# Optimization experiments

Hardware: AMD Instinct MI355X
Metric: run time of the kernel (lower is better)

## Reference

```python
import jax, jax.numpy as jnp
import numpy as np

N, LQ, C = 8, 5440, 256
NH, NL, NP = 8, 4, 4
D_FFN = 1024
SHAPES = np.array([[64, 64], [32, 32], [16, 16], [8, 8]], dtype=np.int32)  # (H, W) per level
assert SHAPES.prod(1).sum() == LQ


def setup_inputs() -> dict:
    key = jax.random.key(0)
    ks = jax.random.split(key, 12)
    s = 0.02
    level_start = np.concatenate([[0], np.cumsum(SHAPES.prod(1))[:-1]]).astype(np.int32)
    return {
        "src": jax.random.normal(ks[0], (N, LQ, C), jnp.float32),
        "pos": jax.random.normal(ks[1], (N, LQ, C), jnp.float32),
        "reference_points": jax.random.uniform(ks[2], (N, LQ, NL, 2), jnp.float32),
        "w_off": jax.random.normal(ks[3], (C, NH * NL * NP * 2), jnp.float32) * s,
        "b_off": jax.random.uniform(ks[4], (NH * NL * NP * 2,), jnp.float32, -0.5, 0.5),
        "w_attn": jax.random.normal(ks[5], (C, NH * NL * NP), jnp.float32) * s,
        "b_attn": jnp.zeros((NH * NL * NP,), jnp.float32),
        "w_val": jax.random.normal(ks[6], (C, C), jnp.float32) * s,
        "b_val": jnp.zeros((C,), jnp.float32),
        "w_out": jax.random.normal(ks[7], (C, C), jnp.float32) * s,
        "b_out": jnp.zeros((C,), jnp.float32),
        "g1": jnp.ones((C,), jnp.float32),
        "be1": jnp.zeros((C,), jnp.float32),
        "w_ff1": jax.random.normal(ks[8], (C, D_FFN), jnp.float32) * s,
        "b_ff1": jnp.zeros((D_FFN,), jnp.float32),
        "w_ff2": jax.random.normal(ks[9], (D_FFN, C), jnp.float32) * s,
        "b_ff2": jnp.zeros((C,), jnp.float32),
        "g2": jnp.ones((C,), jnp.float32),
        "be2": jnp.zeros((C,), jnp.float32),
        "padding_mask": jnp.zeros((N, LQ), bool),
        "spatial_shapes": jnp.asarray(SHAPES),
        "level_start_index": jnp.asarray(level_start),
    }


def _layer_norm(x, g, b, eps=1e-5):
    m = x.mean(-1, keepdims=True)
    v = ((x - m) ** 2).mean(-1, keepdims=True)
    return (x - m) / jnp.sqrt(v + eps) * g + b


def _bilinear(v, gx, gy, Hl, Wl):
    # v: [B, Hl*Wl, D]; gx, gy: [B, Q] normalized grid coords in [-1, 1].
    # Matches F.grid_sample(mode='bilinear', padding_mode='zeros', align_corners=False).
    x = (gx + 1.0) * (Wl * 0.5) - 0.5
    y = (gy + 1.0) * (Hl * 0.5) - 0.5
    x0f, y0f = jnp.floor(x), jnp.floor(y)
    wx, wy = x - x0f, y - y0f
    x0, y0 = x0f.astype(jnp.int32), y0f.astype(jnp.int32)

    def corner(xi, yi, w):
        valid = (xi >= 0) & (xi < Wl) & (yi >= 0) & (yi < Hl)
        idx = jnp.clip(yi, 0, Hl - 1) * Wl + jnp.clip(xi, 0, Wl - 1)
        g = jnp.take_along_axis(v, idx[..., None], axis=1)  # [B, Q, D]
        return g * (w * valid)[..., None]

    return (corner(x0, y0, (1 - wx) * (1 - wy))
            + corner(x0 + 1, y0, wx * (1 - wy))
            + corner(x0, y0 + 1, (1 - wx) * wy)
            + corner(x0 + 1, y0 + 1, wx * wy))


def _forward(src, pos, reference_points, w_off, b_off, w_attn, b_attn, w_val, b_val,
             w_out, b_out, g1, be1, w_ff1, b_ff1, w_ff2, b_ff2, g2, be2, padding_mask):
    D = C // NH
    query = src + pos  # with_pos_embed
    # --- MSDeformAttn ---
    value = src @ w_val + b_val
    value = jnp.where(padding_mask[..., None], 0.0, value).reshape(N, LQ, NH, D)
    off = (query @ w_off + b_off).reshape(N, LQ, NH, NL, NP, 2)
    aw = jax.nn.softmax((query @ w_attn + b_attn).reshape(N, LQ, NH, NL * NP), axis=-1)
    aw = aw.reshape(N, LQ, NH, NL, NP)
    wh = jnp.asarray(SHAPES[:, ::-1].copy(), jnp.float32)  # (W, H) per level
    loc = reference_points[:, :, None, :, None, :] + off / wh[None, None, None, :, None, :]
    out = jnp.zeros((N, LQ, NH, D), src.dtype)
    start = 0
    for l in range(NL):
        Hl, Wl = int(SHAPES[l, 0]), int(SHAPES[l, 1])
        # [N, HW_l, NH, D] -> [N*NH, HW_l, D]
        v = value[:, start:start + Hl * Wl].transpose(0, 2, 1, 3).reshape(N * NH, Hl * Wl, D)
        g = (2.0 * loc[:, :, :, l] - 1.0).transpose(0, 2, 1, 3, 4).reshape(N * NH, LQ * NP, 2)
        samp = _bilinear(v, g[..., 0], g[..., 1], Hl, Wl).reshape(N, NH, LQ, NP, D)
        out = out + jnp.einsum('nhqpd,nqhp->nqhd', samp, aw[:, :, :, l])
        start += Hl * Wl
    src2 = out.reshape(N, LQ, C) @ w_out + b_out
    # --- residual + norm + FFN (dropout = identity in eval) ---
    x = _layer_norm(src + src2, g1, be1)
    h = jax.nn.relu(x @ w_ff1 + b_ff1)
    x = _layer_norm(x + h @ w_ff2 + b_ff2, g2, be2)
    return x


def reference(src, pos, reference_points, w_off, b_off, w_attn, b_attn, w_val, b_val,
              w_out, b_out, g1, be1, w_ff1, b_ff1, w_ff2, b_ff2, g2, be2,
              padding_mask, spatial_shapes, level_start_index):
    return _forward(src, pos, reference_points, w_off, b_off, w_attn, b_attn, w_val, b_val,
                    w_out, b_out, g1, be1, w_ff1, b_ff1, w_ff2, b_ff2, g2, be2, padding_mask)
```

## Files before the change

### kernel.cpp

```cpp
#include <hip/hip_runtime.h>
#include <hip/hip_bf16.h>

typedef __hip_bfloat16 bf16;
typedef __attribute__((ext_vector_type(8))) short short8;
typedef __attribute__((ext_vector_type(4))) float f32x4;

#define NB    8
#define LQ    5440
#define CCH   256
#define NHD   8
#define DFF   1024
#define TT    (NB * LQ)

__device__ __forceinline__ float b2f(bf16 x) { return __bfloat162float(x); }
__device__ __forceinline__ bf16  f2b(float x) { return __float2bfloat16(x); }

__device__ __forceinline__ void gl_lds16(const bf16* g, bf16* l) {
    __builtin_amdgcn_global_load_lds(
        (const __attribute__((address_space(1))) unsigned int*)g,
        (__attribute__((address_space(3))) unsigned int*)l,
        16, 0, 0);
}

template <bool RELU, bool OUT_BF16>
__global__ __launch_bounds__(256) void mfma_gemm(
    const bf16* __restrict__ A, const bf16* __restrict__ BT,
    const float* __restrict__ bias, void* __restrict__ Cout,
    int M, int N, int K)
{
    __shared__ bf16 Abuf[128 * 32];
    __shared__ bf16 Bbuf[128 * 32];

    const int tid = threadIdx.x;
    const int wv = tid >> 6;
    const int ln = tid & 63;
    const int lane15 = ln & 15;
    const int quad = ln >> 4;
    const int m0 = blockIdx.y * 128;
    const int n0 = blockIdx.x * 128;
    const int wm = (wv >> 1) * 64;
    const int wn = (wv & 1) * 64;

    const int ar = tid >> 2;
    const int ac = (tid & 3) * 8;

    const bf16* gA = A  + (size_t)(m0 + ar) * K + ac;
    const bf16* gB = BT + (size_t)(n0 + ar) * K + ac;

    f32x4 acc[4][4];
#pragma unroll
    for (int i = 0; i < 4; i++)
#pragma unroll
        for (int j = 0; j < 4; j++) acc[i][j] = (f32x4){0.f, 0.f, 0.f, 0.f};

    const int KT = K >> 5;
    for (int kt = 0; kt < KT; kt++) {
        const int k0 = kt << 5;
        gl_lds16(gA + k0,                    Abuf + tid * 8);
        gl_lds16(gA + (size_t)64 * K + k0,   Abuf + 2048 + tid * 8);
        gl_lds16(gB + k0,                    Bbuf + tid * 8);
        gl_lds16(gB + (size_t)64 * K + k0,   Bbuf + 2048 + tid * 8);
        __syncthreads();

        short8 afrag[4], bfrag[4];
#pragma unroll
        for (int i = 0; i < 4; i++)
            afrag[i] = *(const short8*)(Abuf + (wm + i * 16 + lane15) * 32 + quad * 8);
#pragma unroll
        for (int i = 0; i < 4; i++)
            bfrag[i] = *(const short8*)(Bbuf + (wn + i * 16 + lane15) * 32 + quad * 8);
#pragma unroll
        for (int mi = 0; mi < 4; mi++)
#pragma unroll
            for (int ni = 0; ni < 4; ni++)
                acc[mi][ni] = __builtin_amdgcn_mfma_f32_16x16x32_bf16(
                    afrag[mi], bfrag[ni], acc[mi][ni], 0, 0, 0);
        __syncthreads();
    }

#pragma unroll
    for (int ni = 0; ni < 4; ni++) {
        const int col = n0 + wn + ni * 16 + lane15;
        const float bi = bias[col];
#pragma unroll
        for (int mi = 0; mi < 4; mi++) {
#pragma unroll
            for (int r = 0; r < 4; r++) {
                const int row = m0 + wm + mi * 16 + quad * 4 + r;
                float v = acc[mi][ni][r] + bi;
                if (RELU) v = v > 0.f ? v : 0.f;
                if (OUT_BF16) ((bf16*)Cout)[(size_t)row * N + col] = f2b(v);
                else          ((float*)Cout)[(size_t)row * N + col] = v;
            }
        }
    }
}

__global__ __launch_bounds__(256) void prep_tokens(
    const float* __restrict__ src, const float* __restrict__ pos,
    bf16* __restrict__ qb, bf16* __restrict__ sb)
{
    const int i = (blockIdx.x * 256 + threadIdx.x) * 4;
    const float4 s = *(const float4*)(src + i);
    const float4 p = *(const float4*)(pos + i);
    union { bf16 h[4]; ushort4 u; } qo, so;
    qo.h[0] = f2b(s.x + p.x); qo.h[1] = f2b(s.y + p.y);
    qo.h[2] = f2b(s.z + p.z); qo.h[3] = f2b(s.w + p.w);
    so.h[0] = f2b(s.x); so.h[1] = f2b(s.y); so.h[2] = f2b(s.z); so.h[3] = f2b(s.w);
    *(ushort4*)(qb + i) = qo.u;
    *(ushort4*)(sb + i) = so.u;
}

__global__ __launch_bounds__(256) void transpose_w(
    const float* __restrict__ W, bf16* __restrict__ WT, int K, int N)
{
    const int i = blockIdx.x * 256 + threadIdx.x;
    if (i >= K * N) return;
    const int n = i / K, k = i - n * K;
    WT[i] = f2b(W[(size_t)k * N + n]);
}

__global__ void concat_bias(const float* __restrict__ b_off,
                            const float* __restrict__ b_attn,
                            float* __restrict__ bqk)
{
    const int i = threadIdx.x;
    if (i < 256) bqk[i] = b_off[i];
    else if (i < 384) bqk[i] = b_attn[i - 256];
}

__global__ __launch_bounds__(256) void msda_kernel(
    const bf16*  __restrict__ value,
    const float* __restrict__ qk,
    const float* __restrict__ refp,
    bf16* __restrict__ outb)
{
    __shared__ uint2 s_ow[8 * 64];

    const int u_local = threadIdx.x >> 5;
    const int unit = blockIdx.x * 8 + u_local;
    const int t = unit >> 3;
    const int h = unit & 7;
    const int lane32 = threadIdx.x & 31;

    if (lane32 < 16) {
        const int p = lane32;
        const int l = p >> 2;
        const int sz = 64 >> l;
        const int starts[4] = {0, 4096, 5120, 5376};

        float logit = qk[(size_t)t * 384 + 256 + h * 16 + p];
        float m = logit;
#pragma unroll
        for (int mk = 1; mk <= 8; mk <<= 1) m = fmaxf(m, __shfl_xor(m, mk));
        const float e = __expf(logit - m);
        float ssum = e;
#pragma unroll
        for (int mk = 1; mk <= 8; mk <<= 1) ssum += __shfl_xor(ssum, mk);
        const float aw = e / ssum;

        const float2 r2 = *(const float2*)(refp + (size_t)t * 8 + l * 2);
        const float2 o2 = *(const float2*)(qk + (size_t)t * 384 + h * 32 + p * 2);
        const float x = r2.x * (float)sz + o2.x - 0.5f;
        const float y = r2.y * (float)sz + o2.y - 0.5f;
        const float x0f = floorf(x), y0f = floorf(y);
        const float wx = x - x0f, wy = y - y0f;
        const int x0 = (int)x0f, y0 = (int)y0f;

        const int n = t / LQ;
        const uint base_tok = (uint)(n * LQ + starts[l]);

        uint2* dst = s_ow + u_local * 64 + p * 4;
#pragma unroll
        for (int cy = 0; cy < 2; cy++) {
            const int yi = y0 + cy;
            const float wyy = cy ? wy : 1.f - wy;
            const bool vy = (yi >= 0) && (yi < sz);
            const int yc = min(max(yi, 0), sz - 1);
#pragma unroll
            for (int cx = 0; cx < 2; cx++) {
                const int xi = x0 + cx;
                const float wxx = cx ? wx : 1.f - wx;
                const bool vx = (xi >= 0) && (xi < sz);
                const int xc = min(max(xi, 0), sz - 1);
                const float w = aw * wxx * wyy * ((vx && vy) ? 1.f : 0.f);
                const uint off = (base_tok + (uint)(yc * sz + xc)) * 256u + (uint)(h * 32);
                dst[cy * 2 + cx] = make_uint2(off, __float_as_uint(w));
            }
        }
    }
    __syncthreads();

    const int d = lane32;
    const uint2* po = s_ow + u_local * 64;
    float acc = 0.f;
#pragma unroll
    for (int c = 0; c < 64; c++) {
        const uint2 ow = po[c];
        acc += __uint_as_float(ow.y) * b2f(value[ow.x + d]);
    }
    outb[(size_t)t * 256 + h * 32 + d] = f2b(acc);
}

template <bool B_BF16, bool WRITE_BF16>
__global__ __launch_bounds__(256) void ln_kernel(
    const float* __restrict__ A, const void* __restrict__ Bv,
    const float* __restrict__ gamma, const float* __restrict__ beta,
    float* __restrict__ outf, bf16* __restrict__ outb)
{
    const int t = blockIdx.x * 4 + (threadIdx.x >> 6);
    const int lane = threadIdx.x & 63;

    float v[4];
    float s = 0.f;
#pragma unroll
    for (int i = 0; i < 4; i++) {
        const int c = lane * 4 + i;
        const float bb = B_BF16 ? b2f(((const bf16*)Bv)[(size_t)t * CCH + c])
                                : ((const float*)Bv)[(size_t)t * CCH + c];
        v[i] = A[(size_t)t * CCH + c] + bb;
        s += v[i];
    }
#pragma unroll
    for (int o = 32; o > 0; o >>= 1) s += __shfl_down(s, o, 64);
    s = __shfl(s, 0, 64);
    const float mean = s * (1.f / 256.f);

    float vs = 0.f;
#pragma unroll
    for (int i = 0; i < 4; i++) { const float dd = v[i] - mean; vs += dd * dd; }
#pragma unroll
    for (int o = 32; o > 0; o >>= 1) vs += __shfl_down(vs, o, 64);
    vs = __shfl(vs, 0, 64);
    const float inv = rsqrtf(vs * (1.f / 256.f) + 1e-5f);

#pragma unroll
    for (int i = 0; i < 4; i++) {
        const int c = lane * 4 + i;
        const float o = (v[i] - mean) * inv * gamma[c] + beta[c];
        outf[(size_t)t * CCH + c] = o;
        if (WRITE_BF16) outb[(size_t)t * CCH + c] = f2b(o);
    }
}

extern "C" void kernel_launch(void* const* d_in, const int* in_sizes, int n_in,
                              void* d_out, int out_size, void* d_ws, size_t ws_size,
                              hipStream_t stream)
{
    const float* src    = (const float*)d_in[0];
    const float* pos    = (const float*)d_in[1];
    const float* refp   = (const float*)d_in[2];
    const float* w_off  = (const float*)d_in[3];
    const float* b_off  = (const float*)d_in[4];
    const float* w_attn = (const float*)d_in[5];
    const float* b_attn = (const float*)d_in[6];
    const float* w_val  = (const float*)d_in[7];
    const float* b_val  = (const float*)d_in[8];
    const float* w_out  = (const float*)d_in[9];
    const float* b_out  = (const float*)d_in[10];
    const float* g1     = (const float*)d_in[11];
    const float* be1    = (const float*)d_in[12];
    const float* w_ff1  = (const float*)d_in[13];
    const float* b_ff1  = (const float*)d_in[14];
    const float* w_ff2  = (const float*)d_in[15];
    const float* b_ff2  = (const float*)d_in[16];
    const float* g2     = (const float*)d_in[17];
    const float* be2    = (const float*)d_in[18];

    float* outp = (float*)d_out;
    char* ws = (char*)d_ws;

    bf16*  q_bf   = (bf16*)(ws);
    bf16*  attn_o = (bf16*)(ws);
    bf16*  s_bf   = (bf16*)(ws + (size_t)TT * 512);
    bf16*  x1b    = (bf16*)(ws + (size_t)TT * 512);
    float* qk_out = (float*)(ws + (size_t)TT * 1024);
    bf16*  ffh    = (bf16*)(ws + (size_t)TT * 1024);
    bf16*  y2b    = (bf16*)(ws + (size_t)TT * 1024 + (size_t)TT * 1024);
    bf16*  value  = (bf16*)(ws + (size_t)TT * 2560);
    float* src2   = (float*)(ws + (size_t)TT * 2560);
    float* x1f    = src2;
    char*  wp     = ws + (size_t)TT * 3584;
    bf16*  wqkT = (bf16*)(wp);
    bf16*  wvT  = (bf16*)(wp + 196608);
    bf16*  woT  = (bf16*)(wp + 327680);
    bf16*  wf1T = (bf16*)(wp + 458752);
    bf16*  wf2T = (bf16*)(wp + 983040);
    float* bqk  = (float*)(wp + 1507328);

    prep_tokens<<<TT * CCH / 4 / 256, 256, 0, stream>>>(src, pos, q_bf, s_bf);
    transpose_w<<<(256 * 256 + 255) / 256, 256, 0, stream>>>(w_off,  wqkT,          256, 256);
    transpose_w<<<(256 * 128 + 255) / 256, 256, 0, stream>>>(w_attn, wqkT + 65536,  256, 128);
    transpose_w<<<(256 * 256 + 255) / 256, 256, 0, stream>>>(w_val,  wvT,           256, 256);
    transpose_w<<<(256 * 256 + 255) / 256, 256, 0, stream>>>(w_out,  woT,           256, 256);
    transpose_w<<<(256 * 1024 + 255) / 256, 256, 0, stream>>>(w_ff1, wf1T,          256, 1024);
    transpose_w<<<(1024 * 256 + 255) / 256, 256, 0, stream>>>(w_ff2, wf2T,          1024, 256);
    concat_bias<<<1, 384, 0, stream>>>(b_off, b_attn, bqk);

    mfma_gemm<false, false><<<dim3(3, TT / 128), 256, 0, stream>>>(
        q_bf, wqkT, bqk, qk_out, TT, 384, 256);
    mfma_gemm<false, true><<<dim3(2, TT / 128), 256, 0, stream>>>(
        s_bf, wvT, b_val, value, TT, 256, 256);
    msda_kernel<<<TT, 256, 0, stream>>>(value, qk_out, refp, attn_o);
    mfma_gemm<false, false><<<dim3(2, TT / 128), 256, 0, stream>>>(
        attn_o, woT, b_out, src2, TT, 256, 256);
    ln_kernel<false, true><<<TT / 4, 256, 0, stream>>>(src, src2, g1, be1, x1f, x1b);

    for (int ch = 0; ch < 2; ch++) {
        const size_t r0 = (size_t)ch * 21760;
        mfma_gemm<true, true><<<dim3(8, 170), 256, 0, stream>>>(
            x1b + r0 * 256, wf1T, b_ff1, ffh, 21760, 1024, 256);
        mfma_gemm<false, true><<<dim3(2, 170), 256, 0, stream>>>(
            ffh, wf2T, b_ff2, y2b + r0 * 256, 21760, 256, 1024);
    }
    ln_kernel<true, false><<<TT / 4, 256, 0, stream>>>(x1f, y2b, g2, be2, outp, nullptr);
}
```

Baseline: 507.4 us.

## Register-prefetch GEMM tiles, readlane-based MSDA, merge weight prep, drop FFN chunking

The GEMM replaces direct global-to-LDS loads with a register prefetch of the next K tile, overlapping global loads with MFMA work. The MSDA kernel drops its shared-memory offset/weight table and broadcasts the per-sample offsets and weights with readlane across a 64-lane wave per (token, head). The six weight-transpose launches and the bias concat become one prep_weights kernel. The FFN is no longer split into two chunks, and the first LayerNorm now writes only a bf16 output, which the second LayerNorm reads back as its residual. That lowers memory traffic but makes the residual path less precise. The MSDA change also doubles the grid and leaves half of each wave idle on the final store.

```diff
diff --git a/kernel.cpp b/kernel.cpp
--- a/kernel.cpp
+++ b/kernel.cpp
@@ -14,13 +14,6 @@
 
 __device__ __forceinline__ float b2f(bf16 x) { return __bfloat162float(x); }
 __device__ __forceinline__ bf16  f2b(float x) { return __float2bfloat16(x); }
-
-__device__ __forceinline__ void gl_lds16(const bf16* g, bf16* l) {
-    __builtin_amdgcn_global_load_lds(
-        (const __attribute__((address_space(1))) unsigned int*)g,
-        (__attribute__((address_space(3))) unsigned int*)l,
-        16, 0, 0);
-}
 
 template <bool RELU, bool OUT_BF16>
 __global__ __launch_bounds__(256) void mfma_gemm(
@@ -44,9 +37,6 @@
     const int ar = tid >> 2;
     const int ac = (tid & 3) * 8;
 
-    const bf16* gA = A  + (size_t)(m0 + ar) * K + ac;
-    const bf16* gB = BT + (size_t)(n0 + ar) * K + ac;
-
     f32x4 acc[4][4];
 #pragma unroll
     for (int i = 0; i < 4; i++)
@@ -54,14 +44,29 @@
         for (int j = 0; j < 4; j++) acc[i][j] = (f32x4){0.f, 0.f, 0.f, 0.f};
 
     const int KT = K >> 5;
+    short8 av[2], bv[2];
+#pragma unroll
+    for (int j = 0; j < 2; j++) {
+        av[j] = *(const short8*)(A  + (size_t)(m0 + j * 64 + ar) * K + ac);
+        bv[j] = *(const short8*)(BT + (size_t)(n0 + j * 64 + ar) * K + ac);
+    }
+
     for (int kt = 0; kt < KT; kt++) {
-        const int k0 = kt << 5;
-        gl_lds16(gA + k0,                    Abuf + tid * 8);
-        gl_lds16(gA + (size_t)64 * K + k0,   Abuf + 2048 + tid * 8);
-        gl_lds16(gB + k0,                    Bbuf + tid * 8);
-        gl_lds16(gB + (size_t)64 * K + k0,   Bbuf + 2048 + tid * 8);
         __syncthreads();
-
+#pragma unroll
+        for (int j = 0; j < 2; j++) {
+            *(short8*)(Abuf + j * 2048 + tid * 8) = av[j];
+            *(short8*)(Bbuf + j * 2048 + tid * 8) = bv[j];
+        }
+        __syncthreads();
+        if (kt + 1 < KT) {
+            const int k0 = (kt + 1) << 5;
+#pragma unroll
+            for (int j = 0; j < 2; j++) {
+                av[j] = *(const short8*)(A  + (size_t)(m0 + j * 64 + ar) * K + k0 + ac);
+                bv[j] = *(const short8*)(BT + (size_t)(n0 + j * 64 + ar) * K + k0 + ac);
+            }
+        }
         short8 afrag[4], bfrag[4];
 #pragma unroll
         for (int i = 0; i < 4; i++)
@@ -75,7 +80,6 @@
             for (int ni = 0; ni < 4; ni++)
                 acc[mi][ni] = __builtin_amdgcn_mfma_f32_16x16x32_bf16(
                     afrag[mi], bfrag[ni], acc[mi][ni], 0, 0, 0);
-        __syncthreads();
     }
 
 #pragma unroll
@@ -111,22 +115,30 @@
     *(ushort4*)(sb + i) = so.u;
 }
 
-__global__ __launch_bounds__(256) void transpose_w(
-    const float* __restrict__ W, bf16* __restrict__ WT, int K, int N)
-{
-    const int i = blockIdx.x * 256 + threadIdx.x;
-    if (i >= K * N) return;
-    const int n = i / K, k = i - n * K;
-    WT[i] = f2b(W[(size_t)k * N + n]);
-}
-
-__global__ void concat_bias(const float* __restrict__ b_off,
-                            const float* __restrict__ b_attn,
-                            float* __restrict__ bqk)
-{
-    const int i = threadIdx.x;
-    if (i < 256) bqk[i] = b_off[i];
-    else if (i < 384) bqk[i] = b_attn[i - 256];
+__global__ __launch_bounds__(256) void prep_weights(
+    const float* __restrict__ w_off, const float* __restrict__ w_attn,
+    const float* __restrict__ w_val, const float* __restrict__ w_out,
+    const float* __restrict__ w_ff1, const float* __restrict__ w_ff2,
+    const float* __restrict__ b_off, const float* __restrict__ b_attn,
+    bf16* __restrict__ wqkT, bf16* __restrict__ wvT, bf16* __restrict__ woT,
+    bf16* __restrict__ wf1T, bf16* __restrict__ wf2T, float* __restrict__ bqk)
+{
+    int i = blockIdx.x * 256 + threadIdx.x;
+    if (i < 65536) {
+        wqkT[i] = f2b(w_off[(size_t)(i & 255) * 256 + (i >> 8)]);
+    } else if ((i -= 65536) < 32768) {
+        wqkT[65536 + i] = f2b(w_attn[(size_t)(i & 255) * 128 + (i >> 8)]);
+    } else if ((i -= 32768) < 65536) {
+        wvT[i] = f2b(w_val[(size_t)(i & 255) * 256 + (i >> 8)]);
+    } else if ((i -= 65536) < 65536) {
+        woT[i] = f2b(w_out[(size_t)(i & 255) * 256 + (i >> 8)]);
+    } else if ((i -= 65536) < 262144) {
+        wf1T[i] = f2b(w_ff1[(size_t)(i & 255) * 1024 + (i >> 8)]);
+    } else if ((i -= 262144) < 262144) {
+        wf2T[i] = f2b(w_ff2[(size_t)(i & 1023) * 256 + (i >> 10)]);
+    } else if ((i -= 262144) < 384) {
+        bqk[i] = (i < 256) ? b_off[i] : b_attn[i - 256];
+    }
 }
 
 __global__ __launch_bounds__(256) void msda_kernel(
@@ -135,78 +147,74 @@
     const float* __restrict__ refp,
     bf16* __restrict__ outb)
 {
-    __shared__ uint2 s_ow[8 * 64];
-
-    const int u_local = threadIdx.x >> 5;
-    const int unit = blockIdx.x * 8 + u_local;
+    const int unit = blockIdx.x * 4 + (threadIdx.x >> 6);
     const int t = unit >> 3;
     const int h = unit & 7;
-    const int lane32 = threadIdx.x & 31;
-
-    if (lane32 < 16) {
-        const int p = lane32;
-        const int l = p >> 2;
-        const int sz = 64 >> l;
-        const int starts[4] = {0, 4096, 5120, 5376};
-
-        float logit = qk[(size_t)t * 384 + 256 + h * 16 + p];
-        float m = logit;
-#pragma unroll
-        for (int mk = 1; mk <= 8; mk <<= 1) m = fmaxf(m, __shfl_xor(m, mk));
-        const float e = __expf(logit - m);
-        float ssum = e;
-#pragma unroll
-        for (int mk = 1; mk <= 8; mk <<= 1) ssum += __shfl_xor(ssum, mk);
-        const float aw = e / ssum;
-
-        const float2 r2 = *(const float2*)(refp + (size_t)t * 8 + l * 2);
-        const float2 o2 = *(const float2*)(qk + (size_t)t * 384 + h * 32 + p * 2);
-        const float x = r2.x * (float)sz + o2.x - 0.5f;
-        const float y = r2.y * (float)sz + o2.y - 0.5f;
-        const float x0f = floorf(x), y0f = floorf(y);
-        const float wx = x - x0f, wy = y - y0f;
-        const int x0 = (int)x0f, y0 = (int)y0f;
-
-        const int n = t / LQ;
-        const uint base_tok = (uint)(n * LQ + starts[l]);
-
-        uint2* dst = s_ow + u_local * 64 + p * 4;
-#pragma unroll
-        for (int cy = 0; cy < 2; cy++) {
-            const int yi = y0 + cy;
-            const float wyy = cy ? wy : 1.f - wy;
-            const bool vy = (yi >= 0) && (yi < sz);
-            const int yc = min(max(yi, 0), sz - 1);
-#pragma unroll
-            for (int cx = 0; cx < 2; cx++) {
-                const int xi = x0 + cx;
-                const float wxx = cx ? wx : 1.f - wx;
-                const bool vx = (xi >= 0) && (xi < sz);
-                const int xc = min(max(xi, 0), sz - 1);
-                const float w = aw * wxx * wyy * ((vx && vy) ? 1.f : 0.f);
-                const uint off = (base_tok + (uint)(yc * sz + xc)) * 256u + (uint)(h * 32);
-                dst[cy * 2 + cx] = make_uint2(off, __float_as_uint(w));
-            }
+    const int lane = threadIdx.x & 63;
+    const int d = lane & 31;
+
+    const int p = lane & 15;
+    const int l = p >> 2;
+    const int sz = 64 >> l;
+    const int start = (16384 - 4 * sz * sz) / 3;
+
+    float logit = qk[(size_t)t * 384 + 256 + h * 16 + p];
+    float mx = logit;
+#pragma unroll
+    for (int mk = 1; mk <= 8; mk <<= 1) mx = fmaxf(mx, __shfl_xor(mx, mk));
+    const float e = __expf(logit - mx);
+    float ssum = e;
+#pragma unroll
+    for (int mk = 1; mk <= 8; mk <<= 1) ssum += __shfl_xor(ssum, mk);
+    const float aw = e / ssum;
+
+    const float2 r2 = *(const float2*)(refp + (size_t)t * 8 + l * 2);
+    const float2 o2 = *(const float2*)(qk + (size_t)t * 384 + h * 32 + p * 2);
+    const float x = r2.x * (float)sz + o2.x - 0.5f;
+    const float y = r2.y * (float)sz + o2.y - 0.5f;
+    const float x0f = floorf(x), y0f = floorf(y);
+    const float wx = x - x0f, wy = y - y0f;
+    const int x0 = (int)x0f, y0 = (int)y0f;
+
+    const uint base_tok = (uint)((t / LQ) * LQ + start);
+
+    uint oo[4];
+    float ww[4];
+#pragma unroll
+    for (int cy = 0; cy < 2; cy++) {
+        const int yi = y0 + cy;
+        const float wyy = cy ? wy : 1.f - wy;
+        const bool vy = (yi >= 0) && (yi < sz);
+        const int yc = min(max(yi, 0), sz - 1);
+#pragma unroll
+        for (int cx = 0; cx < 2; cx++) {
+            const int xi = x0 + cx;
+            const float wxx = cx ? wx : 1.f - wx;
+            const bool vx = (xi >= 0) && (xi < sz);
+            const int xc = min(max(xi, 0), sz - 1);
+            const int j = cy * 2 + cx;
+            ww[j] = aw * wxx * wyy * ((vx && vy) ? 1.f : 0.f);
+            oo[j] = (base_tok + (uint)(yc * sz + xc)) * 256u + (uint)(h * 32);
         }
     }
-    __syncthreads();
-
-    const int d = lane32;
-    const uint2* po = s_ow + u_local * 64;
+
     float acc = 0.f;
 #pragma unroll
     for (int c = 0; c < 64; c++) {
-        const uint2 ow = po[c];
-        acc += __uint_as_float(ow.y) * b2f(value[ow.x + d]);
-    }
-    outb[(size_t)t * 256 + h * 32 + d] = f2b(acc);
-}
-
-template <bool B_BF16, bool WRITE_BF16>
+        const int pp = c >> 2, j = c & 3;
+        const uint  so = (uint)__builtin_amdgcn_readlane((int)oo[j], pp);
+        const float sw = __int_as_float(
+            __builtin_amdgcn_readlane(__float_as_int(ww[j]), pp));
+        acc = fmaf(sw, b2f(value[(size_t)so + d]), acc);
+    }
+    if (lane < 32) outb[(size_t)t * 256 + h * 32 + d] = f2b(acc);
+}
+
+template <bool A_BF16, bool B_BF16, bool OUT_BF16>
 __global__ __launch_bounds__(256) void ln_kernel(
-    const float* __restrict__ A, const void* __restrict__ Bv,
+    const void* __restrict__ Av, const void* __restrict__ Bv,
     const float* __restrict__ gamma, const float* __restrict__ beta,
-    float* __restrict__ outf, bf16* __restrict__ outb)
+    void* __restrict__ outv)
 {
     const int t = blockIdx.x * 4 + (threadIdx.x >> 6);
     const int lane = threadIdx.x & 63;
@@ -216,9 +224,11 @@
 #pragma unroll
     for (int i = 0; i < 4; i++) {
         const int c = lane * 4 + i;
+        const float aa = A_BF16 ? b2f(((const bf16*)Av)[(size_t)t * CCH + c])
+                                : ((const float*)Av)[(size_t)t * CCH + c];
         const float bb = B_BF16 ? b2f(((const bf16*)Bv)[(size_t)t * CCH + c])
                                 : ((const float*)Bv)[(size_t)t * CCH + c];
-        v[i] = A[(size_t)t * CCH + c] + bb;
+        v[i] = aa + bb;
         s += v[i];
     }
 #pragma unroll
@@ -238,8 +248,8 @@
     for (int i = 0; i < 4; i++) {
         const int c = lane * 4 + i;
         const float o = (v[i] - mean) * inv * gamma[c] + beta[c];
-        outf[(size_t)t * CCH + c] = o;
-        if (WRITE_BF16) outb[(size_t)t * CCH + c] = f2b(o);
+        if (OUT_BF16) ((bf16*)outv)[(size_t)t * CCH + c] = f2b(o);
+        else          ((float*)outv)[(size_t)t * CCH + c] = o;
     }
 }
 
@@ -275,11 +285,10 @@
     bf16*  s_bf   = (bf16*)(ws + (size_t)TT * 512);
     bf16*  x1b    = (bf16*)(ws + (size_t)TT * 512);
     float* qk_out = (float*)(ws + (size_t)TT * 1024);
+    float* src2   = (float*)(ws + (size_t)TT * 1024);
     bf16*  ffh    = (bf16*)(ws + (size_t)TT * 1024);
-    bf16*  y2b    = (bf16*)(ws + (size_t)TT * 1024 + (size_t)TT * 1024);
     bf16*  value  = (bf16*)(ws + (size_t)TT * 2560);
-    float* src2   = (float*)(ws + (size_t)TT * 2560);
-    float* x1f    = src2;
+    bf16*  y2b    = (bf16*)(ws + (size_t)TT * 3072);
     char*  wp     = ws + (size_t)TT * 3584;
     bf16*  wqkT = (bf16*)(wp);
     bf16*  wvT  = (bf16*)(wp + 196608);
@@ -289,29 +298,22 @@
     float* bqk  = (float*)(wp + 1507328);
 
     prep_tokens<<<TT * CCH / 4 / 256, 256, 0, stream>>>(src, pos, q_bf, s_bf);
-    transpose_w<<<(256 * 256 + 255) / 256, 256, 0, stream>>>(w_off,  wqkT,          256, 256);
-    transpose_w<<<(256 * 128 + 255) / 256, 256, 0, stream>>>(w_attn, wqkT + 65536,  256, 128);
-    transpose_w<<<(256 * 256 + 255) / 256, 256, 0, stream>>>(w_val,  wvT,           256, 256);
-    transpose_w<<<(256 * 256 + 255) / 256, 256, 0, stream>>>(w_out,  woT,           256, 256);
-    transpose_w<<<(256 * 1024 + 255) / 256, 256, 0, stream>>>(w_ff1, wf1T,          256, 1024);
-    transpose_w<<<(1024 * 256 + 255) / 256, 256, 0, stream>>>(w_ff2, wf2T,          1024, 256);
-    concat_bias<<<1, 384, 0, stream>>>(b_off, b_attn, bqk);
+    prep_weights<<<(753664 + 384 + 255) / 256, 256, 0, stream>>>(
+        w_off, w_attn, w_val, w_out, w_ff1, w_ff2, b_off, b_attn,
+        wqkT, wvT, woT, wf1T, wf2T, bqk);
 
     mfma_gemm<false, false><<<dim3(3, TT / 128), 256, 0, stream>>>(
         q_bf, wqkT, bqk, qk_out, TT, 384, 256);
     mfma_gemm<false, true><<<dim3(2, TT / 128), 256, 0, stream>>>(
         s_bf, wvT, b_val, value, TT, 256, 256);
-    msda_kernel<<<TT, 256, 0, stream>>>(value, qk_out, refp, attn_o);
+    msda_kernel<<<TT * 2, 256, 0, stream>>>(value, qk_out, refp, attn_o);
     mfma_gemm<false, false><<<dim3(2, TT / 128), 256, 0, stream>>>(
         attn_o, woT, b_out, src2, TT, 256, 256);
-    ln_kernel<false, true><<<TT / 4, 256, 0, stream>>>(src, src2, g1, be1, x1f, x1b);
-
-    for (int ch = 0; ch < 2; ch++) {
-        const size_t r0 = (size_t)ch * 21760;
-        mfma_gemm<true, true><<<dim3(8, 170), 256, 0, stream>>>(
-            x1b + r0 * 256, wf1T, b_ff1, ffh, 21760, 1024, 256);
-        mfma_gemm<false, true><<<dim3(2, 170), 256, 0, stream>>>(
-            ffh, wf2T, b_ff2, y2b + r0 * 256, 21760, 256, 1024);
-    }
-    ln_kernel<true, false><<<TT / 4, 256, 0, stream>>>(x1f, y2b, g2, be2, outp, nullptr);
-}
+    ln_kernel<false, false, true><<<TT / 4, 256, 0, stream>>>(src, src2, g1, be1, x1b);
+
+    mfma_gemm<true, true><<<dim3(8, TT / 128), 256, 0, stream>>>(
+        x1b, wf1T, b_ff1, ffh, TT, 1024, 256);
+    mfma_gemm<false, true><<<dim3(2, TT / 128), 256, 0, stream>>>(
+        ffh, wf2T, b_ff2, y2b, TT, 256, 1024);
+    ln_kernel<true, true, false><<<TT / 4, 256, 0, stream>>>(x1b, y2b, g2, be2, outp);
+}
```

Result: slower. 643.6 us (+26.8%).
